# Kernel tuning notes

Hardware: AMD Instinct MI355X
Metric: run time of the kernel (lower is better)

Reference implementation:

```python
import jax, jax.numpy as jnp
import numpy as np

N_NODES = 100000
N_EDGES = 1600000
IN_CH, HID_CH, OUT_CH = 128, 64, 32


def glorot(key, shape):
    lim = np.sqrt(6.0 / (shape[0] + shape[1]))
    return jax.random.uniform(key, shape, jnp.float32, -lim, lim)


def setup_inputs() -> dict:
    key = jax.random.key(0)
    k_x, k_e, k_w1, k_w2 = jax.random.split(key, 4)
    x = jax.random.normal(k_x, (N_NODES, IN_CH), dtype=jnp.float32)
    edge_index = jax.random.randint(k_e, (2, N_EDGES), 0, N_NODES, dtype=jnp.int64)
    return {
        "x": x,
        "edge_index": edge_index,
        "W1": glorot(k_w1, (IN_CH, HID_CH)),
        "b1": jnp.zeros((HID_CH,), jnp.float32),
        "W2": glorot(k_w2, (HID_CH, OUT_CH)),
        "b2": jnp.zeros((OUT_CH,), jnp.float32),
    }


def gcn_conv(x, src, dst, W, b):
    """PyG GCNConv: add self-loops, symmetric D^-1/2 (A+I) D^-1/2 normalization.
    Messages flow src -> dst. Linear transform applied before aggregation."""
    n = x.shape[0]
    h = x @ W  # [N, out]
    # degree including self-loop
    deg = jnp.zeros((n,), h.dtype).at[dst].add(1.0) + 1.0
    dinv = jax.lax.rsqrt(deg)
    norm = dinv[src] * dinv[dst]  # [E]
    # neighbor aggregation (scatter-add) + self-loop contribution (norm = dinv_i^2)
    agg = jnp.zeros_like(h).at[dst].add(h[src] * norm[:, None])
    agg = agg + h * (dinv * dinv)[:, None]
    return agg + b


def reference(x, edge_index, W1, b1, W2, b2):
    src, dst = edge_index[0], edge_index[1]
    h = jax.nn.relu(gcn_conv(x, src, dst, W1, b1))
    return gcn_conv(h, src, dst, W2, b2)
```

## Files before the change

### kernel.cpp

```cpp
#include <hip/hip_runtime.h>
#include <hip/hip_fp16.h>


#define N_NODES 100000
#define N_EDGES 1600000
#define BSHIFT 8
#define NBUCK ((N_NODES + 255) / 256)
#define CAP 5120
#define CSRCAP 6656
#define EPB 1024
#define NBLKA ((N_EDGES + EPB - 1) / EPB)

__global__ __launch_bounds__(256) void k_init(int* gfix, __half* h1s, __half* h2s) {
    int i = blockIdx.x * 256 + threadIdx.x;
    if (i < NBUCK) gfix[i] = i * CAP;
    if (blockIdx.x == 1) {
        int t = threadIdx.x;
        if (t < 32) ((unsigned*)(h1s + (size_t)N_NODES * 64))[t] = 0u;
        else if (t < 48) ((unsigned*)(h2s + (size_t)N_NODES * 32))[t - 32] = 0u;
    }
}

__global__ __launch_bounds__(256) void k_bucketA(const int* __restrict__ src,
                                                 const int* __restrict__ dst,
                                                 int* gfix, int2* __restrict__ tmp) {
    __shared__ int lcnt[NBUCK];
    __shared__ int lpos[NBUCK];
    int t = threadIdx.x;
    for (int b = t; b < NBUCK; b += 256) lcnt[b] = 0;
    __syncthreads();
    long e0 = (long)blockIdx.x * EPB;
    #pragma unroll
    for (int k = 0; k < EPB / 256; ++k) {
        long e = e0 + k * 256 + t;
        if (e < N_EDGES) atomicAdd(&lcnt[dst[e] >> BSHIFT], 1);
    }
    __syncthreads();
    for (int b = t; b < NBUCK; b += 256) {
        int c = lcnt[b];
        lpos[b] = c ? atomicAdd(&gfix[b], c) : 0;
    }
    __syncthreads();
    #pragma unroll
    for (int k = 0; k < EPB / 256; ++k) {
        long e = e0 + k * 256 + t;
        if (e < N_EDGES) {
            int d = dst[e];
            int bkt = d >> BSHIFT;
            int p = atomicAdd(&lpos[bkt], 1);
            if (p < bkt * CAP + CAP)
                tmp[p] = (int2){d, src[e]};
        }
    }
}

__global__ __launch_bounds__(256) void k_bucketB(const int* __restrict__ gfix,
                                                 const int2* __restrict__ tmp,
                                                 int* __restrict__ rowstart,
                                                 int* __restrict__ udeg,
                                                 float* __restrict__ dinv,
                                                 int* __restrict__ csr) {
    __shared__ int cnt[256];
    __shared__ int s[256];
    __shared__ int cur[256];
    __shared__ int rsl[256];
    int b  = blockIdx.x;
    int t  = threadIdx.x;
    int n0 = b << BSHIFT;
    int nn = min(256, N_NODES - n0);
    cnt[t] = 0;
    __syncthreads();
    int start = b * CAP;
    int end   = min(gfix[b], start + CAP);
    for (int e = start + t; e < end; e += 256)
        atomicAdd(&cnt[tmp[e].x - n0], 1);
    __syncthreads();
    int c   = (t < nn) ? cnt[t] : 0;
    int pad = (c + 15) & ~15;
    s[t] = pad;
    __syncthreads();
    for (int off = 1; off < 256; off <<= 1) {
        int add = (t >= off) ? s[t - off] : 0;
        __syncthreads();
        s[t] += add;
        __syncthreads();
    }
    int rs = b * CSRCAP + s[t] - pad;
    rsl[t] = rs;
    cur[t] = rs;
    if (t < nn) {
        rowstart[n0 + t] = rs;
        udeg[n0 + t]     = c;
        dinv[n0 + t]     = rsqrtf((float)(c + 1));
    }
    __syncthreads();
    for (int e = start + t; e < end; e += 256) {
        int2 p = tmp[e];
        int pos = atomicAdd(&cur[p.x - n0], 1);
        csr[pos] = p.y;
    }
    __syncthreads();
    int pe = rsl[t] + pad;
    for (int p = cur[t]; p < pe; ++p) csr[p] = N_NODES;
}

__global__ __launch_bounds__(256) void k_gemm1(const float* __restrict__ x,
                                               const float* __restrict__ W1,
                                               const float* __restrict__ dinv,
                                               __half* __restrict__ h1s) {
    __shared__ float Ws[128 * 64];
    __shared__ float xs[16][132];
    int tid = threadIdx.x;
    for (int i = tid * 4; i < 128 * 64; i += 1024)
        *(float4*)&Ws[i] = *(const float4*)&W1[i];
    long rowBase = (long)blockIdx.x * 16;
    for (int i = tid; i < 512; i += 256) {
        int r = i >> 5, c4 = i & 31;
        *(float4*)&xs[r][c4 * 4] = *(const float4*)&x[(rowBase + r) * 128 + c4 * 4];
    }
    __syncthreads();
    int r  = tid >> 4;
    int cg = (tid & 15) * 4;
    float a0 = 0, a1 = 0, a2 = 0, a3 = 0;
    #pragma unroll
    for (int k = 0; k < 128; ++k) {
        float xv = xs[r][k];
        const float* w = &Ws[k * 64 + cg];
        a0 = fmaf(xv, w[0], a0); a1 = fmaf(xv, w[1], a1);
        a2 = fmaf(xv, w[2], a2); a3 = fmaf(xv, w[3], a3);
    }
    long row = rowBase + r;
    float dv = dinv[row];
    ushort4 pk;
    pk.x = __half_as_ushort(__float2half_rn(a0 * dv));
    pk.y = __half_as_ushort(__float2half_rn(a1 * dv));
    pk.z = __half_as_ushort(__float2half_rn(a2 * dv));
    pk.w = __half_as_ushort(__float2half_rn(a3 * dv));
    *(ushort4*)&h1s[row * 64 + cg] = pk;
}

__global__ __launch_bounds__(256) void k_fused1(const int* __restrict__ rowstart,
                                                const int* __restrict__ udeg,
                                                const int* __restrict__ csr,
                                                const float* __restrict__ dinv,
                                                const __half* __restrict__ h1s,
                                                const float* __restrict__ b1,
                                                const float* __restrict__ W2,
                                                __half* __restrict__ h2s) {
    __shared__ float W2s[64 * 32];
    __shared__ float g1row[4][72];
    int tid = threadIdx.x;
    for (int idx = tid * 4; idx < 64 * 32; idx += 1024)
        *(float4*)&W2s[idx] = *(const float4*)&W2[idx];
    __syncthreads();
    int w = tid >> 6, c = tid & 63;
    int pr = c >> 4, hc = c & 15;
    int i = blockIdx.x * 4 + w;
    int n = udeg[i];
    int base = rowstart[i];
    float4 acc = {0.f, 0.f, 0.f, 0.f};
    if (pr == 0) {
        uint2 v = *(const uint2*)(h1s + (size_t)i * 64 + hc * 4);
        float2 a = __half22float2(*(__half2*)&v.x);
        float2 b = __half22float2(*(__half2*)&v.y);
        acc.x = a.x; acc.y = a.y; acc.z = b.x; acc.w = b.y;
    }
    for (int k = 0; k < n; k += 16) {
        int4 ia = *(const int4*)&csr[base + k];
        int4 ib = *(const int4*)&csr[base + k + 4];
        int4 ic = *(const int4*)&csr[base + k + 8];
        int4 id = *(const int4*)&csr[base + k + 12];
        int s0, s1, s2, s3;
        switch (pr) {
            case 0:  s0 = ia.x; s1 = ib.x; s2 = ic.x; s3 = id.x; break;
            case 1:  s0 = ia.y; s1 = ib.y; s2 = ic.y; s3 = id.y; break;
            case 2:  s0 = ia.z; s1 = ib.z; s2 = ic.z; s3 = id.z; break;
            default: s0 = ia.w; s1 = ib.w; s2 = ic.w; s3 = id.w; break;
        }
        uint2 v0 = *(const uint2*)(h1s + (size_t)s0 * 64 + hc * 4);
        uint2 v1 = *(const uint2*)(h1s + (size_t)s1 * 64 + hc * 4);
        uint2 v2 = *(const uint2*)(h1s + (size_t)s2 * 64 + hc * 4);
        uint2 v3 = *(const uint2*)(h1s + (size_t)s3 * 64 + hc * 4);
        float2 a0 = __half22float2(*(__half2*)&v0.x), b0 = __half22float2(*(__half2*)&v0.y);
        float2 a1 = __half22float2(*(__half2*)&v1.x), b1f = __half22float2(*(__half2*)&v1.y);
        float2 a2 = __half22float2(*(__half2*)&v2.x), b2f = __half22float2(*(__half2*)&v2.y);
        float2 a3 = __half22float2(*(__half2*)&v3.x), b3f = __half22float2(*(__half2*)&v3.y);
        acc.x += (a0.x + a1.x) + (a2.x + a3.x);
        acc.y += (a0.y + a1.y) + (a2.y + a3.y);
        acc.z += (b0.x + b1f.x) + (b2f.x + b3f.x);
        acc.w += (b0.y + b1f.y) + (b2f.y + b3f.y);
    }
    acc.x += __shfl_xor(acc.x, 16); acc.y += __shfl_xor(acc.y, 16);
    acc.z += __shfl_xor(acc.z, 16); acc.w += __shfl_xor(acc.w, 16);
    acc.x += __shfl_xor(acc.x, 32); acc.y += __shfl_xor(acc.y, 32);
    acc.z += __shfl_xor(acc.z, 32); acc.w += __shfl_xor(acc.w, 32);
    float dvi = dinv[i];
    if (pr == 0) {
        float4 bb = *(const float4*)&b1[hc * 4];
        float4 g;
        g.x = fmaxf(fmaf(dvi, acc.x, bb.x), 0.f);
        g.y = fmaxf(fmaf(dvi, acc.y, bb.y), 0.f);
        g.z = fmaxf(fmaf(dvi, acc.z, bb.z), 0.f);
        g.w = fmaxf(fmaf(dvi, acc.w, bb.w), 0.f);
        *(float4*)&g1row[w][hc * 4] = g;
    }
    int j = c & 31, hf = c >> 5;
    float dot = 0.f;
    #pragma unroll
    for (int cc = 0; cc < 32; ++cc)
        dot = fmaf(g1row[w][hf * 32 + cc], W2s[(hf * 32 + cc) * 32 + j], dot);
    dot += __shfl_xor(dot, 32);
    if (hf == 0)
        h2s[(size_t)i * 32 + j] = __float2half_rn(dot * dvi);
}

__global__ __launch_bounds__(256) void k_gather2(const int* __restrict__ rowstart,
                                                 const int* __restrict__ udeg,
                                                 const int* __restrict__ csr,
                                                 const float* __restrict__ dinv,
                                                 const __half* __restrict__ h2s,
                                                 const float* __restrict__ b2,
                                                 float* __restrict__ out) {
    int tid = threadIdx.x;
    int w = tid >> 6, c = tid & 63;
    int pr = c >> 3, hc = c & 7;
    int i = blockIdx.x * 4 + w;
    int n = udeg[i];
    int base = rowstart[i];
    float4 acc = {0.f, 0.f, 0.f, 0.f};
    if (pr == 0) {
        uint2 v = *(const uint2*)(h2s + (size_t)i * 32 + hc * 4);
        float2 a = __half22float2(*(__half2*)&v.x);
        float2 b = __half22float2(*(__half2*)&v.y);
        acc.x = a.x; acc.y = a.y; acc.z = b.x; acc.w = b.y;
    }
    for (int k = 0; k < n; k += 16) {
        int4 ia = *(const int4*)&csr[base + k];
        int4 ib = *(const int4*)&csr[base + k + 4];
        int4 ic = *(const int4*)&csr[base + k + 8];
        int4 id = *(const int4*)&csr[base + k + 12];
        int s0, s1;
        switch (pr) {
            case 0:  s0 = ia.x; s1 = ic.x; break;
            case 1:  s0 = ia.y; s1 = ic.y; break;
            case 2:  s0 = ia.z; s1 = ic.z; break;
            case 3:  s0 = ia.w; s1 = ic.w; break;
            case 4:  s0 = ib.x; s1 = id.x; break;
            case 5:  s0 = ib.y; s1 = id.y; break;
            case 6:  s0 = ib.z; s1 = id.z; break;
            default: s0 = ib.w; s1 = id.w; break;
        }
        uint2 v0 = *(const uint2*)(h2s + (size_t)s0 * 32 + hc * 4);
        uint2 v1 = *(const uint2*)(h2s + (size_t)s1 * 32 + hc * 4);
        float2 a0 = __half22float2(*(__half2*)&v0.x), b0 = __half22float2(*(__half2*)&v0.y);
        float2 a1 = __half22float2(*(__half2*)&v1.x), b1f = __half22float2(*(__half2*)&v1.y);
        acc.x += a0.x + a1.x; acc.y += a0.y + a1.y;
        acc.z += b0.x + b1f.x; acc.w += b0.y + b1f.y;
    }
    acc.x += __shfl_xor(acc.x, 8);  acc.y += __shfl_xor(acc.y, 8);
    acc.z += __shfl_xor(acc.z, 8);  acc.w += __shfl_xor(acc.w, 8);
    acc.x += __shfl_xor(acc.x, 16); acc.y += __shfl_xor(acc.y, 16);
    acc.z += __shfl_xor(acc.z, 16); acc.w += __shfl_xor(acc.w, 16);
    acc.x += __shfl_xor(acc.x, 32); acc.y += __shfl_xor(acc.y, 32);
    acc.z += __shfl_xor(acc.z, 32); acc.w += __shfl_xor(acc.w, 32);
    if (pr == 0) {
        float dvi = dinv[i];
        float4 bb = *(const float4*)&b2[hc * 4];
        float4 o;
        o.x = fmaf(dvi, acc.x, bb.x);
        o.y = fmaf(dvi, acc.y, bb.y);
        o.z = fmaf(dvi, acc.z, bb.z);
        o.w = fmaf(dvi, acc.w, bb.w);
        *(float4*)&out[(size_t)i * 32 + hc * 4] = o;
    }
}

extern "C" void kernel_launch(void* const* d_in, const int* in_sizes, int n_in,
                              void* d_out, int out_size, void* d_ws, size_t ws_size,
                              hipStream_t stream) {
    const float* x  = (const float*)d_in[0];
    const int*   ei = (const int*)d_in[1];
    const float* W1 = (const float*)d_in[2];
    const float* b1 = (const float*)d_in[3];
    const float* W2 = (const float*)d_in[4];
    const float* b2 = (const float*)d_in[5];
    float* out = (float*)d_out;

    const int* src = ei;
    const int* dst = ei + N_EDGES;

    char* ws = (char*)d_ws;
    const size_t MB = 1u << 20;
    int*    udeg     = (int*)   (ws + 0);
    float*  dinv     = (float*) (ws + 512 * 1024);
    int*    rowstart = (int*)   (ws + 1 * MB);
    int*    gfix     = (int*)   (ws + 1 * MB + 512 * 1024);
    int*    csr      = (int*)   (ws + 2 * MB);
    int2*   tmp      = (int2*)  (ws + 13 * MB);
    __half* h1s      = (__half*)(ws + 30 * MB);
    __half* h2s      = (__half*)(ws + 43 * MB);

    k_init   <<<2, 256, 0, stream>>>(gfix, h1s, h2s);
    k_bucketA<<<NBLKA, 256, 0, stream>>>(src, dst, gfix, tmp);
    k_bucketB<<<NBUCK, 256, 0, stream>>>(gfix, tmp, rowstart, udeg, dinv, csr);
    k_gemm1  <<<N_NODES / 16, 256, 0, stream>>>(x, W1, dinv, h1s);
    k_fused1 <<<N_NODES / 4, 256, 0, stream>>>(rowstart, udeg, csr, dinv, h1s, b1, W2, h2s);
    k_gather2<<<N_NODES / 4, 256, 0, stream>>>(rowstart, udeg, csr, dinv, h2s, b2, out);
}
```

Measured before the change: 300.1 us.

## Pack bucket entries into 32 bits and use per-wave histograms in bucketing

Intermediate bucket entries are packed into one 32-bit word holding the low 8 bits of dst and a 17-bit src, replacing the previous int2. This halves tmp traffic in both bucketing kernels. Edges per block are doubled, and each wavefront keeps its own shared histogram, which cuts shared-atomic contention and lets dst/src be held in registers instead of reloaded. The cost is more global atomics on gfix, since each wave reserves its own slots, and more shared memory per block.

```diff
diff --git a/kernel.cpp b/kernel.cpp
--- a/kernel.cpp
+++ b/kernel.cpp
@@ -8,7 +8,7 @@
 #define NBUCK ((N_NODES + 255) / 256)
 #define CAP 5120
 #define CSRCAP 6656
-#define EPB 1024
+#define EPB 2048
 #define NBLKA ((N_EDGES + EPB - 1) / EPB)
 
 __global__ __launch_bounds__(256) void k_init(int* gfix, __half* h1s, __half* h2s) {
@@ -23,39 +23,41 @@
 
 __global__ __launch_bounds__(256) void k_bucketA(const int* __restrict__ src,
                                                  const int* __restrict__ dst,
-                                                 int* gfix, int2* __restrict__ tmp) {
-    __shared__ int lcnt[NBUCK];
-    __shared__ int lpos[NBUCK];
-    int t = threadIdx.x;
-    for (int b = t; b < NBUCK; b += 256) lcnt[b] = 0;
+                                                 int* gfix, unsigned* __restrict__ tmp) {
+    __shared__ int lcnt[4][NBUCK];
+    __shared__ int lpos[4][NBUCK];
+    int t = threadIdx.x, w = t >> 6, lane = t & 63;
+    for (int b = lane; b < NBUCK; b += 64) lcnt[w][b] = 0;
     __syncthreads();
     long e0 = (long)blockIdx.x * EPB;
+    int d[8], s[8];
     #pragma unroll
-    for (int k = 0; k < EPB / 256; ++k) {
+    for (int k = 0; k < 8; ++k) {
         long e = e0 + k * 256 + t;
-        if (e < N_EDGES) atomicAdd(&lcnt[dst[e] >> BSHIFT], 1);
-    }
-    __syncthreads();
-    for (int b = t; b < NBUCK; b += 256) {
-        int c = lcnt[b];
-        lpos[b] = c ? atomicAdd(&gfix[b], c) : 0;
+        bool v = e < N_EDGES;
+        d[k] = v ? dst[e] : -1;
+        s[k] = v ? src[e] : 0;
+        if (v) atomicAdd(&lcnt[w][d[k] >> BSHIFT], 1);
+    }
+    __syncthreads();
+    for (int b = lane; b < NBUCK; b += 64) {
+        int c = lcnt[w][b];
+        lpos[w][b] = c ? atomicAdd(&gfix[b], c) : 0;
     }
     __syncthreads();
     #pragma unroll
-    for (int k = 0; k < EPB / 256; ++k) {
-        long e = e0 + k * 256 + t;
-        if (e < N_EDGES) {
-            int d = dst[e];
-            int bkt = d >> BSHIFT;
-            int p = atomicAdd(&lpos[bkt], 1);
+    for (int k = 0; k < 8; ++k) {
+        if (d[k] >= 0) {
+            int bkt = d[k] >> BSHIFT;
+            int p = atomicAdd(&lpos[w][bkt], 1);
             if (p < bkt * CAP + CAP)
-                tmp[p] = (int2){d, src[e]};
+                tmp[p] = ((unsigned)(d[k] & 255) << 17) | (unsigned)s[k];
         }
     }
 }
 
 __global__ __launch_bounds__(256) void k_bucketB(const int* __restrict__ gfix,
-                                                 const int2* __restrict__ tmp,
+                                                 const unsigned* __restrict__ tmp,
                                                  int* __restrict__ rowstart,
                                                  int* __restrict__ udeg,
                                                  float* __restrict__ dinv,
@@ -73,7 +75,7 @@
     int start = b * CAP;
     int end   = min(gfix[b], start + CAP);
     for (int e = start + t; e < end; e += 256)
-        atomicAdd(&cnt[tmp[e].x - n0], 1);
+        atomicAdd(&cnt[tmp[e] >> 17], 1);
     __syncthreads();
     int c   = (t < nn) ? cnt[t] : 0;
     int pad = (c + 15) & ~15;
@@ -95,9 +97,9 @@
     }
     __syncthreads();
     for (int e = start + t; e < end; e += 256) {
-        int2 p = tmp[e];
-        int pos = atomicAdd(&cur[p.x - n0], 1);
-        csr[pos] = p.y;
+        unsigned p = tmp[e];
+        int pos = atomicAdd(&cur[p >> 17], 1);
+        csr[pos] = (int)(p & 0x1FFFFu);
     }
     __syncthreads();
     int pe = rsl[t] + pad;
@@ -291,14 +293,14 @@
 
     char* ws = (char*)d_ws;
     const size_t MB = 1u << 20;
-    int*    udeg     = (int*)   (ws + 0);
-    float*  dinv     = (float*) (ws + 512 * 1024);
-    int*    rowstart = (int*)   (ws + 1 * MB);
-    int*    gfix     = (int*)   (ws + 1 * MB + 512 * 1024);
-    int*    csr      = (int*)   (ws + 2 * MB);
-    int2*   tmp      = (int2*)  (ws + 13 * MB);
-    __half* h1s      = (__half*)(ws + 30 * MB);
-    __half* h2s      = (__half*)(ws + 43 * MB);
+    int*      udeg     = (int*)     (ws + 0);
+    float*    dinv     = (float*)   (ws + 512 * 1024);
+    int*      rowstart = (int*)     (ws + 1 * MB);
+    int*      gfix     = (int*)     (ws + 1 * MB + 512 * 1024);
+    int*      csr      = (int*)     (ws + 2 * MB);
+    unsigned* tmp      = (unsigned*)(ws + 13 * MB);
+    __half*   h1s      = (__half*)  (ws + 22 * MB);
+    __half*   h2s      = (__half*)  (ws + 35 * MB);
 
     k_init   <<<2, 256, 0, stream>>>(gfix, h1s, h2s);
     k_bucketA<<<NBLKA, 256, 0, stream>>>(src, dst, gfix, tmp);
```

Result: slower. 374.3 us (+24.7%).
